# Kernel tuning notes

Hardware: AMD Instinct MI355X
Metric: run time of the kernel (lower is better)

The kernel has to match this reference:

```python
import jax, jax.numpy as jnp
import numpy as np

T, INPUT, RES = 8192, 1024, 4096


def setup_inputs() -> dict:
    key = jax.random.key(0)
    k1, k2, k3 = jax.random.split(key, 3)
    x = jax.random.normal(k1, (T, INPUT, 1), dtype=jnp.float32)
    # nn.init.uniform_(a=-1, b=1)
    W_in = jax.random.uniform(k2, (RES, INPUT), dtype=jnp.float32, minval=-1.0, maxval=1.0)
    # diagonal of W_res: uniform(-spectral_radius, spectral_radius), spectral_radius=1.0
    d = jax.random.uniform(k3, (RES,), dtype=jnp.float32, minval=-1.0, maxval=1.0)
    return {"x": x, "W_in": W_in, "d": d}


def reference(x, W_in, d):
    # Precompute input projection for all timesteps: [T, RES]
    # (the per-step W_in @ x_t hoisted out of the sequential loop)
    U = jnp.einsum('ri,ti->tr', W_in, x[:, :, 0])

    # W_res is diagonal, so W_res @ state == d * state (elementwise).
    def step(s, u):
        s_new = jnp.tanh(u + d * s)
        return s_new, s_new

    s0 = jnp.zeros((RES,), dtype=x.dtype)  # initial state (torch.zeros)
    _, states = jax.lax.scan(step, s0, U)  # states: [T, RES]
    return states[:, :, None]  # torch.unsqueeze(states, -1) -> [T, RES, 1]
```

## Files before the change

### kernel.cpp

```cpp
#include <hip/hip_runtime.h>
#include <hip/hip_bf16.h>

#define T_DIM 8192
#define IN_DIM 1024
#define RES_DIM 4096

typedef unsigned short u16;
typedef _Float16 f16;
typedef f16 f16x8 __attribute__((ext_vector_type(8)));
typedef float f32x4 __attribute__((ext_vector_type(4)));
typedef float f32x16 __attribute__((ext_vector_type(16)));

__device__ __forceinline__ float tanh_fast(float z) {
    z = fminf(15.0f, fmaxf(-15.0f, z));
    float e = __expf(2.0f * z);
    float inv = __builtin_amdgcn_rcpf(e + 1.0f);
    return fmaf(-2.0f, inv, 1.0f);
}

__device__ __forceinline__ void stage16(const u16* g, u16* l) {
    __builtin_amdgcn_global_load_lds(
        (const __attribute__((address_space(1))) void*)g,
        (__attribute__((address_space(3))) void*)l, 16, 0, 0);
}

__global__ void convert_all(const float* __restrict__ x, const float* __restrict__ Wsrc,
                            u16* __restrict__ Xh, u16* __restrict__ Xl,
                            u16* __restrict__ Wf, int nX, int nTot) {
    for (int g = blockIdx.x * blockDim.x + threadIdx.x; g < nTot;
         g += gridDim.x * blockDim.x) {
        const int isX = (g < nX);
        const int c   = isX ? g : (g - nX);
        int row = c & 127;
        int kq  = (c >> 7) & 3;
        int kt  = (c >> 9) & 31;
        int rt  = c >> 14;
        const float* src = (isX ? x : Wsrc) + (size_t)(rt * 128 + row) * 1024 + kt * 32 + kq * 8;
        float4 f0 = *(const float4*)src;
        float4 f1 = *(const float4*)(src + 4);
        float f[8] = {f0.x, f0.y, f0.z, f0.w, f1.x, f1.y, f1.z, f1.w};
        alignas(16) u16 hv[8];
        alignas(16) u16 lv[8];
#pragma unroll
        for (int e = 0; e < 8; ++e) {
            f16 h = (f16)f[e];
            f16 l = (f16)(f[e] - (float)h);
            hv[e] = *(const u16*)&h;
            lv[e] = *(const u16*)&l;
        }
        if (isX) {
            *(uint4*)(Xh + (size_t)c * 8) = *(const uint4*)hv;
            *(uint4*)(Xl + (size_t)c * 8) = *(const uint4*)lv;
        } else {
            *(uint4*)(Wf + (size_t)c * 8) = *(const uint4*)hv;
        }
    }
}

__global__ __launch_bounds__(256, 2)
void gemm_f16_wide2(const u16* __restrict__ Xh, const u16* __restrict__ Xl,
                    const u16* __restrict__ Wf, float* __restrict__ C) {
    __shared__ __attribute__((aligned(16))) u16 sAh[2][4096];
    __shared__ __attribute__((aligned(16))) u16 sAl[2][4096];
    __shared__ __attribute__((aligned(16))) u16 sW[2][2][4096];

    const int tid  = threadIdx.x;
    const int lane = tid & 63;
    const int wave = tid >> 6;
    const int wr = wave >> 1, wc = wave & 1;
    const int bm = blockIdx.x, bn = blockIdx.y;

    f32x16 acc[2][4] = {};

    const int l31 = lane & 31;
    const int kgl = lane >> 5;

    for (int ktp = 0; ktp < 16; ++ktp) {
        __syncthreads();
#pragma unroll
        for (int s = 0; s < 2; ++s) {
            const int kt = ktp * 2 + s;
            const u16* gX0 = Xh + ((size_t)(bm * 32 + kt)) * 4096;
            const u16* gX1 = Xl + ((size_t)(bm * 32 + kt)) * 4096;
            const u16* gW0 = Wf + ((size_t)((bn * 2 + 0) * 32 + kt)) * 4096;
            const u16* gW1 = Wf + ((size_t)((bn * 2 + 1) * 32 + kt)) * 4096;
#pragma unroll
            for (int i = 0; i < 2; ++i) {
                int off = i * 2048 + tid * 8;
                int wb  = i * 2048 + (tid & ~63) * 8;
                stage16(gX0 + off, &sAh[s][0] + wb);
                stage16(gX1 + off, &sAl[s][0] + wb);
                stage16(gW0 + off, &sW[s][0][0] + wb);
                stage16(gW1 + off, &sW[s][1][0] + wb);
            }
        }
        __syncthreads();

#pragma unroll
        for (int s = 0; s < 2; ++s) {
            f16x8 ah[2][2], al8[2][2], bw[4][2];
#pragma unroll
            for (int mf = 0; mf < 2; ++mf)
#pragma unroll
                for (int ks = 0; ks < 2; ++ks) {
                    int ao = (ks * 2 + kgl) * 1024 + (wr * 64 + mf * 32 + l31) * 8;
                    ah[mf][ks]  = *(const f16x8*)(&sAh[s][0] + ao);
                    al8[mf][ks] = *(const f16x8*)(&sAl[s][0] + ao);
                }
#pragma unroll
            for (int nf = 0; nf < 4; ++nf)
#pragma unroll
                for (int ks = 0; ks < 2; ++ks) {
                    int bo = (ks * 2 + kgl) * 1024 + (nf * 32 + l31) * 8;
                    bw[nf][ks] = *(const f16x8*)(&sW[s][wc][0] + bo);
                }
#pragma unroll
            for (int mf = 0; mf < 2; ++mf)
#pragma unroll
                for (int nf = 0; nf < 4; ++nf)
#pragma unroll
                    for (int ks = 0; ks < 2; ++ks) {
                        acc[mf][nf] = __builtin_amdgcn_mfma_f32_32x32x16_f16(
                            ah[mf][ks], bw[nf][ks], acc[mf][nf], 0, 0, 0);
                        acc[mf][nf] = __builtin_amdgcn_mfma_f32_32x32x16_f16(
                            al8[mf][ks], bw[nf][ks], acc[mf][nf], 0, 0, 0);
                    }
        }
    }

    const size_t t0 = (size_t)bm * 128 + wr * 64;
    const size_t c0 = (size_t)bn * 256 + wc * 128;
#pragma unroll
    for (int mf = 0; mf < 2; ++mf)
#pragma unroll
        for (int nf = 0; nf < 4; ++nf) {
            float* cp = C + (t0 + mf * 32) * RES_DIM + (c0 + nf * 32 + l31);
#pragma unroll
            for (int r = 0; r < 16; ++r) {
                int row = (r & 3) + 8 * (r >> 2) + 4 * kgl;
                cp[(size_t)row * RES_DIM] = acc[mf][nf][r];
            }
        }
}

__global__ __launch_bounds__(256)
void gemm_f32(const float* __restrict__ A, const float* __restrict__ B, float* __restrict__ C) {
    __shared__ float sAf[64][33];
    __shared__ float sBf[64][33];
    const int tid = threadIdx.x;
    const int tx = tid & 15, ty = tid >> 4;
    const size_t t0 = (size_t)blockIdx.x * 64;
    const size_t r0 = (size_t)blockIdx.y * 64;
    const int lrow = tid >> 2;
    const int lcol = (tid & 3) * 8;
    float acc[4][4] = {};
    for (int k0 = 0; k0 < IN_DIM; k0 += 32) {
        float4 a0 = *(const float4*)&A[(t0 + lrow) * IN_DIM + k0 + lcol];
        float4 a1 = *(const float4*)&A[(t0 + lrow) * IN_DIM + k0 + lcol + 4];
        float4 b0 = *(const float4*)&B[(r0 + lrow) * IN_DIM + k0 + lcol];
        float4 b1 = *(const float4*)&B[(r0 + lrow) * IN_DIM + k0 + lcol + 4];
        __syncthreads();
        sAf[lrow][lcol + 0] = a0.x; sAf[lrow][lcol + 1] = a0.y;
        sAf[lrow][lcol + 2] = a0.z; sAf[lrow][lcol + 3] = a0.w;
        sAf[lrow][lcol + 4] = a1.x; sAf[lrow][lcol + 5] = a1.y;
        sAf[lrow][lcol + 6] = a1.z; sAf[lrow][lcol + 7] = a1.w;
        sBf[lrow][lcol + 0] = b0.x; sBf[lrow][lcol + 1] = b0.y;
        sBf[lrow][lcol + 2] = b0.z; sBf[lrow][lcol + 3] = b0.w;
        sBf[lrow][lcol + 4] = b1.x; sBf[lrow][lcol + 5] = b1.y;
        sBf[lrow][lcol + 6] = b1.z; sBf[lrow][lcol + 7] = b1.w;
        __syncthreads();
#pragma unroll
        for (int kk = 0; kk < 32; ++kk) {
            float av[4], bv[4];
#pragma unroll
            for (int i = 0; i < 4; ++i) av[i] = sAf[ty * 4 + i][kk];
#pragma unroll
            for (int j = 0; j < 4; ++j) bv[j] = sBf[tx * 4 + j][kk];
#pragma unroll
            for (int i = 0; i < 4; ++i)
#pragma unroll
                for (int j = 0; j < 4; ++j) acc[i][j] = fmaf(av[i], bv[j], acc[i][j]);
        }
    }
#pragma unroll
    for (int i = 0; i < 4; ++i)
#pragma unroll
        for (int j = 0; j < 4; ++j)
            C[(t0 + ty * 4 + i) * RES_DIM + r0 + tx * 4 + j] = acc[i][j];
}

__global__ void warmup2_kernel(const float* __restrict__ U, const float* __restrict__ d,
                               float* __restrict__ sinit, int C, int W, int NC) {
    int g = blockIdx.x * blockDim.x + threadIdx.x;
    if (g >= NC * (RES_DIM / 2)) return;
    int c = g >> 11;
    int r2 = g & 2047;
    float2 s = make_float2(0.0f, 0.0f);
    if (c > 0) {
        float2 dr = ((const float2*)d)[r2];
        const float2* p = (const float2*)U + (size_t)(c * C - W) * 2048 + r2;
        constexpr int PF = 8;
        float2 buf[PF];
#pragma unroll
        for (int i = 0; i < PF; ++i) buf[i] = p[(size_t)i * 2048];
        for (int t = 0; t < W; t += PF) {
#pragma unroll
            for (int j = 0; j < PF; ++j) {
                float2 u = buf[j];
                int tn = t + j + PF;
                if (tn < W) buf[j] = p[(size_t)tn * 2048];
                s.x = tanh_fast(fmaf(dr.x, s.x, u.x));
                s.y = tanh_fast(fmaf(dr.y, s.y, u.y));
            }
        }
    }
    ((float2*)sinit)[g] = s;
}

__global__ void scan2_kernel(float* __restrict__ U, const float* __restrict__ d,
                             const float* __restrict__ sinit, int C, int NC) {
    int g = blockIdx.x * blockDim.x + threadIdx.x;
    if (g >= NC * (RES_DIM / 2)) return;
    int c = g >> 11;
    int r2 = g & 2047;
    float2 dr = ((const float2*)d)[r2];
    float2 s = (c == 0) ? make_float2(0.0f, 0.0f) : ((const float2*)sinit)[g];
    float2* p = (float2*)U + (size_t)c * C * 2048 + r2;
    constexpr int PF = 8;
    float2 buf[PF];
#pragma unroll
    for (int i = 0; i < PF; ++i) buf[i] = p[(size_t)i * 2048];
    for (int t = 0; t < C; t += PF) {
#pragma unroll
        for (int j = 0; j < PF; ++j) {
            float2 u = buf[j];
            int tn = t + j + PF;
            if (tn < C) buf[j] = p[(size_t)tn * 2048];
            s.x = tanh_fast(fmaf(dr.x, s.x, u.x));
            s.y = tanh_fast(fmaf(dr.y, s.y, u.y));
            p[(size_t)(t + j) * 2048] = s;
        }
    }
}

extern "C" void kernel_launch(void* const* d_in, const int* in_sizes, int n_in,
                              void* d_out, int out_size, void* d_ws, size_t ws_size,
                              hipStream_t stream) {
    const float* x    = (const float*)d_in[0];
    const float* W_in = (const float*)d_in[1];
    const float* dvec = (const float*)d_in[2];
    float* out = (float*)d_out;

    constexpr int NC   = 64;
    constexpr int CHK  = T_DIM / NC;
    constexpr int WARM = 64;

    const size_t szX = (size_t)T_DIM * IN_DIM * sizeof(u16);
    const size_t szW = (size_t)RES_DIM * IN_DIM * sizeof(u16);
    const size_t szS = (size_t)NC * RES_DIM * sizeof(float);

    if (ws_size >= 2 * szX + szW + szS) {
        u16* Xh = (u16*)d_ws;
        u16* Xl = Xh + (size_t)T_DIM * IN_DIM;
        u16* Wf = Xl + (size_t)T_DIM * IN_DIM;
        float* sinit = (float*)(Wf + (size_t)RES_DIM * IN_DIM);

        const int nX   = T_DIM * IN_DIM / 8;
        const int nTot = nX + RES_DIM * IN_DIM / 8;
        convert_all<<<3072, 256, 0, stream>>>(x, W_in, Xh, Xl, Wf, nX, nTot);
        gemm_f16_wide2<<<dim3(T_DIM / 128, RES_DIM / 256), 256, 0, stream>>>(Xh, Xl, Wf, out);
        warmup2_kernel<<<NC * (RES_DIM / 2) / 256, 256, 0, stream>>>(out, dvec, sinit, CHK, WARM, NC);
        scan2_kernel<<<NC * (RES_DIM / 2) / 256, 256, 0, stream>>>(out, dvec, sinit, CHK, NC);
    } else {
        gemm_f32<<<dim3(T_DIM / 64, RES_DIM / 64), 256, 0, stream>>>(x, W_in, out);
        if (ws_size >= szS) {
            float* sinit = (float*)d_ws;
            warmup2_kernel<<<NC * (RES_DIM / 2) / 256, 256, 0, stream>>>(out, dvec, sinit, CHK, WARM, NC);
            scan2_kernel<<<NC * (RES_DIM / 2) / 256, 256, 0, stream>>>(out, dvec, sinit, CHK, NC);
        } else {
            scan2_kernel<<<(RES_DIM / 2) / 256, 256, 0, stream>>>(out, dvec, nullptr, T_DIM, 1);
        }
    }
}
```

Before: 205.9 us.

## Double-buffer LDS staging in f16 GEMM to overlap loads with MFMA

The GEMM main loop now prefetches the next K-tile into the alternate LDS buffer while running MFMAs on the current one, with one barrier per K-tile. Previously each iteration loaded two K-tiles, waited for them, then computed on both, so loads and compute within a block never overlapped. The launch-bounds minimum of two blocks per CU is also dropped. That lets the compiler use more registers, which may lower occupancy and reduce the cross-block latency hiding the old version relied on.

```diff
diff --git a/kernel.cpp b/kernel.cpp
--- a/kernel.cpp
+++ b/kernel.cpp
@@ -57,9 +57,9 @@
     }
 }
 
-__global__ __launch_bounds__(256, 2)
-void gemm_f16_wide2(const u16* __restrict__ Xh, const u16* __restrict__ Xl,
-                    const u16* __restrict__ Wf, float* __restrict__ C) {
+__global__ __launch_bounds__(256)
+void gemm_f16_dbuf(const u16* __restrict__ Xh, const u16* __restrict__ Xl,
+                   const u16* __restrict__ Wf, float* __restrict__ C) {
     __shared__ __attribute__((aligned(16))) u16 sAh[2][4096];
     __shared__ __attribute__((aligned(16))) u16 sAl[2][4096];
     __shared__ __attribute__((aligned(16))) u16 sW[2][2][4096];
@@ -75,58 +75,59 @@
     const int l31 = lane & 31;
     const int kgl = lane >> 5;
 
-    for (int ktp = 0; ktp < 16; ++ktp) {
+#define STAGE(kt, d) do {                                                     \
+    const u16* gX0_ = Xh + ((size_t)(bm * 32 + (kt))) * 4096;                 \
+    const u16* gX1_ = Xl + ((size_t)(bm * 32 + (kt))) * 4096;                 \
+    const u16* gW0_ = Wf + ((size_t)((bn * 2 + 0) * 32 + (kt))) * 4096;       \
+    const u16* gW1_ = Wf + ((size_t)((bn * 2 + 1) * 32 + (kt))) * 4096;       \
+    _Pragma("unroll") for (int i_ = 0; i_ < 2; ++i_) {                        \
+        int off_ = i_ * 2048 + tid * 8;                                       \
+        int wb_  = i_ * 2048 + (tid & ~63) * 8;                               \
+        stage16(gX0_ + off_, &sAh[d][0] + wb_);                               \
+        stage16(gX1_ + off_, &sAl[d][0] + wb_);                               \
+        stage16(gW0_ + off_, &sW[d][0][0] + wb_);                             \
+        stage16(gW1_ + off_, &sW[d][1][0] + wb_);                             \
+    } } while (0)
+
+    STAGE(0, 0);
+    __syncthreads();
+
+#pragma unroll 1
+    for (int kt = 0; kt < 32; ++kt) {
+        const int cur = kt & 1;
+        if (kt + 1 < 32) STAGE(kt + 1, cur ^ 1);
+
+        f16x8 ah[2][2], al8[2][2], bw[4][2];
+#pragma unroll
+        for (int mf = 0; mf < 2; ++mf)
+#pragma unroll
+            for (int ks = 0; ks < 2; ++ks) {
+                int ao = (ks * 2 + kgl) * 1024 + (wr * 64 + mf * 32 + l31) * 8;
+                ah[mf][ks]  = *(const f16x8*)(&sAh[cur][0] + ao);
+                al8[mf][ks] = *(const f16x8*)(&sAl[cur][0] + ao);
+            }
+#pragma unroll
+        for (int nf = 0; nf < 4; ++nf)
+#pragma unroll
+            for (int ks = 0; ks < 2; ++ks) {
+                int bo = (ks * 2 + kgl) * 1024 + (nf * 32 + l31) * 8;
+                bw[nf][ks] = *(const f16x8*)(&sW[cur][wc][0] + bo);
+            }
+#pragma unroll
+        for (int mf = 0; mf < 2; ++mf)
+#pragma unroll
+            for (int nf = 0; nf < 4; ++nf)
+#pragma unroll
+                for (int ks = 0; ks < 2; ++ks) {
+                    acc[mf][nf] = __builtin_amdgcn_mfma_f32_32x32x16_f16(
+                        ah[mf][ks], bw[nf][ks], acc[mf][nf], 0, 0, 0);
+                    acc[mf][nf] = __builtin_amdgcn_mfma_f32_32x32x16_f16(
+                        al8[mf][ks], bw[nf][ks], acc[mf][nf], 0, 0, 0);
+                }
+
         __syncthreads();
-#pragma unroll
-        for (int s = 0; s < 2; ++s) {
-            const int kt = ktp * 2 + s;
-            const u16* gX0 = Xh + ((size_t)(bm * 32 + kt)) * 4096;
-            const u16* gX1 = Xl + ((size_t)(bm * 32 + kt)) * 4096;
-            const u16* gW0 = Wf + ((size_t)((bn * 2 + 0) * 32 + kt)) * 4096;
-            const u16* gW1 = Wf + ((size_t)((bn * 2 + 1) * 32 + kt)) * 4096;
-#pragma unroll
-            for (int i = 0; i < 2; ++i) {
-                int off = i * 2048 + tid * 8;
-                int wb  = i * 2048 + (tid & ~63) * 8;
-                stage16(gX0 + off, &sAh[s][0] + wb);
-                stage16(gX1 + off, &sAl[s][0] + wb);
-                stage16(gW0 + off, &sW[s][0][0] + wb);
-                stage16(gW1 + off, &sW[s][1][0] + wb);
-            }
-        }
-        __syncthreads();
-
-#pragma unroll
-        for (int s = 0; s < 2; ++s) {
-            f16x8 ah[2][2], al8[2][2], bw[4][2];
-#pragma unroll
-            for (int mf = 0; mf < 2; ++mf)
-#pragma unroll
-                for (int ks = 0; ks < 2; ++ks) {
-                    int ao = (ks * 2 + kgl) * 1024 + (wr * 64 + mf * 32 + l31) * 8;
-                    ah[mf][ks]  = *(const f16x8*)(&sAh[s][0] + ao);
-                    al8[mf][ks] = *(const f16x8*)(&sAl[s][0] + ao);
-                }
-#pragma unroll
-            for (int nf = 0; nf < 4; ++nf)
-#pragma unroll
-                for (int ks = 0; ks < 2; ++ks) {
-                    int bo = (ks * 2 + kgl) * 1024 + (nf * 32 + l31) * 8;
-                    bw[nf][ks] = *(const f16x8*)(&sW[s][wc][0] + bo);
-                }
-#pragma unroll
-            for (int mf = 0; mf < 2; ++mf)
-#pragma unroll
-                for (int nf = 0; nf < 4; ++nf)
-#pragma unroll
-                    for (int ks = 0; ks < 2; ++ks) {
-                        acc[mf][nf] = __builtin_amdgcn_mfma_f32_32x32x16_f16(
-                            ah[mf][ks], bw[nf][ks], acc[mf][nf], 0, 0, 0);
-                        acc[mf][nf] = __builtin_amdgcn_mfma_f32_32x32x16_f16(
-                            al8[mf][ks], bw[nf][ks], acc[mf][nf], 0, 0, 0);
-                    }
-        }
-    }
+    }
+#undef STAGE
 
     const size_t t0 = (size_t)bm * 128 + wr * 64;
     const size_t c0 = (size_t)bn * 256 + wc * 128;
@@ -268,7 +269,7 @@
         const int nX   = T_DIM * IN_DIM / 8;
         const int nTot = nX + RES_DIM * IN_DIM / 8;
         convert_all<<<3072, 256, 0, stream>>>(x, W_in, Xh, Xl, Wf, nX, nTot);
-        gemm_f16_wide2<<<dim3(T_DIM / 128, RES_DIM / 256), 256, 0, stream>>>(Xh, Xl, Wf, out);
+        gemm_f16_dbuf<<<dim3(T_DIM / 128, RES_DIM / 256), 256, 0, stream>>>(Xh, Xl, Wf, out);
         warmup2_kernel<<<NC * (RES_DIM / 2) / 256, 256, 0, stream>>>(out, dvec, sinit, CHK, WARM, NC);
         scan2_kernel<<<NC * (RES_DIM / 2) / 256, 256, 0, stream>>>(out, dvec, sinit, CHK, NC);
     } else {
```

Result: slower. 213.0 us (+3.4%).
